# Optimization experiments

Hardware: AMD Instinct MI355X
Metric: run time of the kernel (lower is better)

Reference implementation:

```python
import jax, jax.numpy as jnp
import numpy as np

CH = 64          # channels
OC = 64          # out_channels
B, H, W = 8, 128, 128
NCA_C = CH + OC  # 128, NCA state channels
K = 3            # kernel_size
DILS = (1, 2, 4, 8)
HID = 64         # NCA update hidden
EPS = 1e-5


def setup_inputs() -> dict:
    key = jax.random.key(0)
    ks = jax.random.split(key, 16)
    def n(k, shape, s=0.02):
        return jax.random.normal(k, shape, jnp.float32) * s
    return {
        "x": jax.random.normal(ks[0], (B, H, W, CH), jnp.float32),
        "c": jax.random.normal(ks[1], (B, OC), jnp.float32),
        # Attention params
        "Wq": n(ks[2], (CH, OC)), "bq": jnp.zeros((OC,), jnp.float32),
        "Wk": n(ks[3], (OC, OC)), "bk": jnp.zeros((OC,), jnp.float32),
        "Wv": n(ks[4], (OC, OC)), "bv": jnp.zeros((OC,), jnp.float32),
        "Wo": n(ks[5], (OC, OC)), "bo": jnp.zeros((OC,), jnp.float32),
        "ln_g": jnp.ones((OC,), jnp.float32), "ln_b": jnp.zeros((OC,), jnp.float32),
        # NCA depthwise perception kernels, one per dilation: [4, NCA_C, 1, K, K]
        "pk": n(ks[6], (len(DILS), NCA_C, 1, K, K), 0.1),
        # NCA update MLP
        "W1": n(ks[7], ((1 + len(DILS)) * NCA_C, HID)), "b1": jnp.zeros((HID,), jnp.float32),
        "W2": n(ks[8], (HID, CH)), "b2": jnp.zeros((CH,), jnp.float32),
    }


def _layernorm(z, g, b):
    m = jnp.mean(z, axis=-1, keepdims=True)
    v = jnp.var(z, axis=-1, keepdims=True)
    return (z - m) / jnp.sqrt(v + EPS) * g + b


def _forward(x, c, Wq, bq, Wk, bk, Wv, bv, Wo, bo, ln_g, ln_b, pk, W1, b1, W2, b2):
    b_, h_, w_, _ = x.shape
    # ---- Attention(x, c): single-key softmax pooling over H*W ----
    q = x.reshape(b_, h_ * w_, CH) @ Wq + bq              # [B, HW, OC]
    k = c @ Wk + bk                                        # [B, OC]
    v = c @ Wv + bv                                        # [B, OC]
    scores = jnp.einsum('bno,bo->bn', q, k) * (OC ** -0.5)  # [B, HW]
    attn = jax.nn.softmax(scores, axis=1)                  # softmax over spatial dim
    attended = jnp.einsum('bn,bo->bo', attn, v)            # weighted pool (weights sum to 1)
    a = _layernorm(attended @ Wo + bo + c, ln_g, ln_b)     # out_proj + residual + LN
    c2 = c + a                                             # outer residual in NCAAttention

    # ---- concat broadcast context -> NCA state [B,H,W,NCA_C] ----
    c_exp = jnp.broadcast_to(c2[:, None, None, :], (b_, h_, w_, OC))
    xc = jnp.concatenate([x, c_exp], axis=-1)

    # ---- NCA perception: depthwise dilated convs (SAME padding) ----
    xp = jnp.transpose(xc, (0, 3, 1, 2))                   # NCHW
    feats = [xc]
    for i, d in enumerate(DILS):
        pad = d * (K // 2)
        p = jax.lax.conv_general_dilated(
            xp, pk[i], window_strides=(1, 1),
            padding=[(pad, pad), (pad, pad)], rhs_dilation=(d, d),
            dimension_numbers=('NCHW', 'OIHW', 'NCHW'),
            feature_group_count=NCA_C)
        feats.append(jnp.transpose(p, (0, 2, 3, 1)))
    upd_in = jnp.concatenate(feats, axis=-1)               # [B,H,W,5*NCA_C]

    # ---- NCA update MLP: Linear -> (Dropout=id) -> GELU -> Linear ----
    hidden = jax.nn.gelu(upd_in @ W1 + b1, approximate=False)
    y = hidden @ W2 + b2                                   # [B,H,W,CH]
    # NCA.out_channels (64) != NCA.channels (128) -> no residual add
    return y, c2


def reference(x, c, Wq, bq, Wk, bk, Wv, bv, Wo, bo, ln_g, ln_b, pk, W1, b1, W2, b2):
    return _forward(x, c, Wq, bq, Wk, bk, Wv, bv, Wo, bo, ln_g, ln_b, pk, W1, b1, W2, b2)
```

## Files before the change

### kernel.cpp

```cpp
#include <hip/hip_runtime.h>
#include <hip/hip_bf16.h>
#include <math.h>


typedef float  f32x4 __attribute__((ext_vector_type(4)));
typedef short  s16x8 __attribute__((ext_vector_type(8)));
typedef long   i64x2 __attribute__((ext_vector_type(2)));

static __device__ __forceinline__ unsigned short f2bf(float f) {
    __hip_bfloat16 h = __float2bfloat16(f);
    unsigned short u; __builtin_memcpy(&u, &h, 2); return u;
}
static __device__ __forceinline__ unsigned pk4fp8(float f0, float f1, float f2, float f3) {
    int v = 0;
    v = __builtin_amdgcn_cvt_pk_fp8_f32(f0, f1, v, false);
    v = __builtin_amdgcn_cvt_pk_fp8_f32(f2, f3, v, true);
    return (unsigned)v;
}

#define XROWB  9216
#define XBATCH 1327104
#define USCALE 256.0f

__global__ void prep1(const float* __restrict__ c,
                      const float* __restrict__ Wv, const float* __restrict__ bv,
                      const float* __restrict__ Wo, const float* __restrict__ bo,
                      const float* __restrict__ lng, const float* __restrict__ lnb,
                      float* __restrict__ c2f, float* __restrict__ outc2)
{
    const int b = blockIdx.x, j = threadIdx.x;
    __shared__ float sc[64], sv[64];
    float cj = c[b*64 + j];
    sc[j] = cj; __syncthreads();
    float v = bv[j];
    for (int i = 0; i < 64; ++i) v += sc[i]*Wv[i*64 + j];
    sv[j] = v; __syncthreads();
    float t = bo[j] + cj;
    for (int i = 0; i < 64; ++i) t += sv[i]*Wo[i*64 + j];
    float s = t;
    for (int o = 32; o > 0; o >>= 1) s += __shfl_xor(s, o);
    float m = s * (1.f/64.f);
    float dq = (t - m)*(t - m);
    for (int o = 32; o > 0; o >>= 1) dq += __shfl_xor(dq, o);
    float a = (t - m) / sqrtf(dq*(1.f/64.f) + 1e-5f) * lng[j] + lnb[j];
    float c2 = cj + a;
    c2f[b*64 + j] = c2;
    outc2[b*64 + j] = c2;
}

__global__ void prep2(const float* __restrict__ x,  const float* __restrict__ pk,
                      const float* __restrict__ W1, const float* __restrict__ W2,
                      const float* __restrict__ b1, const float* __restrict__ c2f,
                      unsigned char* __restrict__ xp, unsigned char* __restrict__ Uf,
                      unsigned short* __restrict__ W2s,
                      float* __restrict__ V, float* __restrict__ hcp)
{
    const int blk = blockIdx.x, tid = threadIdx.x;
    if (blk < 512) {
        int i = blk*256 + tid;
        int xc = i & 127, y = (i >> 7) & 127, b = i >> 14;
        const float* src = x + (size_t)i*64;
        float4 f[16];
        #pragma unroll
        for (int k = 0; k < 16; ++k) f[k] = *(const float4*)(src + k*4);
        unsigned P[16];
        #pragma unroll
        for (int k = 0; k < 16; ++k) P[k] = pk4fp8(f[k].x, f[k].y, f[k].z, f[k].w);
        unsigned char* d = xp + (size_t)b*XBATCH + (size_t)(y+8)*XROWB + (size_t)(xc+8)*64;
        *(uint4*)(d +  0) = make_uint4(P[0], P[1], P[8],  P[9]);
        *(uint4*)(d + 16) = make_uint4(P[2], P[3], P[10], P[11]);
        *(uint4*)(d + 32) = make_uint4(P[4], P[5], P[12], P[13]);
        *(uint4*)(d + 48) = make_uint4(P[6], P[7], P[14], P[15]);
    } else if (blk < 648) {
        int idx = (blk - 512)*256 + tid;
        int b = idx / 4352, r = idx - b*4352;
        int yy, xx;
        if (r < 2304) { int ry = r / 144; xx = r - ry*144; yy = (ry < 8) ? ry : 128 + ry; }
        else { int r2 = r - 2304; yy = 8 + (r2 >> 4); int xi = r2 & 15; xx = (xi < 8) ? xi : 128 + xi; }
        unsigned char* d = xp + (size_t)b*XBATCH + (size_t)yy*XROWB + (size_t)xx*64;
        uint4 z = make_uint4(0,0,0,0);
        *(uint4*)(d) = z; *(uint4*)(d+16) = z; *(uint4*)(d+32) = z; *(uint4*)(d+48) = z;
    } else if (blk < 681) {
        int idx = (blk - 648)*256 + tid;
        if (idx < 8448) {
            int lane = idx & 63, nt = (idx >> 6) & 3, pos = idx >> 8;
            int n  = nt*16 + (lane & 15);
            static constexpr int DI[33] = {3,3,3, 2,2,2, 1,1,1, 0,0,0, -1, 0,0, 1,1, 2,2, 3,3,
                                           0,0,0, 1,1,1, 2,2,2, 3,3,3};
            static constexpr int TT[33] = {0,1,2, 0,1,2, 0,1,2, 0,1,2, 4, 3,5, 3,5, 3,5, 3,5,
                                           6,7,8, 6,7,8, 6,7,8, 6,7,8};
            int di = DI[pos], t = TT[pos];
            float vv[16];
            #pragma unroll
            for (int kc2 = 0; kc2 < 2; ++kc2)
                #pragma unroll
                for (int j = 0; j < 8; ++j) {
                    int ch = kc2*32 + (lane >> 4)*8 + j;
                    float v;
                    if (di < 0) {
                        v = W1[ch*64 + n];
                        for (int dd = 0; dd < 4; ++dd)
                            v += pk[(dd*128 + ch)*9 + 4] * W1[((1+dd)*128 + ch)*64 + n];
                    } else {
                        v = pk[(di*128 + ch)*9 + t] * W1[((1+di)*128 + ch)*64 + n];
                    }
                    vv[kc2*8 + j] = v * USCALE;
                }
            uint4 o;
            o.x = pk4fp8(vv[0],  vv[1],  vv[2],  vv[3]);
            o.y = pk4fp8(vv[4],  vv[5],  vv[6],  vv[7]);
            o.z = pk4fp8(vv[8],  vv[9],  vv[10], vv[11]);
            o.w = pk4fp8(vv[12], vv[13], vv[14], vv[15]);
            *(uint4*)(Uf + (size_t)idx*16) = o;
        }
    } else if (blk < 683) {
        int idx = (blk - 681)*256 + tid;
        int lane = idx & 63, nt = (idx >> 6) & 3, kc2 = (idx >> 8) & 1;
        int n  = nt*16 + (lane & 15);
        int k0 = kc2*32 + (lane >> 4)*8;
        unsigned short e[8];
        #pragma unroll
        for (int j = 0; j < 8; ++j) e[j] = f2bf(W2[(k0+j)*64 + n]);
        uint4 o;
        o.x = (unsigned)e[0] | ((unsigned)e[1] << 16);
        o.y = (unsigned)e[2] | ((unsigned)e[3] << 16);
        o.z = (unsigned)e[4] | ((unsigned)e[5] << 16);
        o.w = (unsigned)e[6] | ((unsigned)e[7] << 16);
        *(uint4*)(W2s + (size_t)idx*8) = o;
    } else if (blk < 755) {
        int idx = (blk - 683)*256 + tid;
        int n = idx & 63, q = idx >> 6;
        int p = q % 36, b = q / 36;
        int di = p/9, t = p%9;
        float s = 0.f;
        for (int j = 0; j < 64; ++j)
            s += c2f[b*64 + j] * pk[(di*128 + 64 + j)*9 + t] * W1[((1+di)*128 + 64 + j)*64 + n];
        V[(size_t)q*64 + n] = s;
    } else {
        for (int it = tid; it < 512; it += 256) {
            int b = it >> 6, n = it & 63;
            float s = b1[n];
            for (int j = 0; j < 64; ++j) s += c2f[b*64 + j]*W1[(64 + j)*64 + n];
            hcp[it] = s;
        }
    }
}

#define HID_S 72

__global__ __launch_bounds__(256) void nca_main(
    const unsigned char* __restrict__ xp,
    const unsigned char* __restrict__ U,
    const unsigned short* __restrict__ W2s,
    const float* __restrict__ V,
    const float* __restrict__ hcp,
    const float* __restrict__ b2,
    float* __restrict__ out)
{
    __shared__ unsigned short hid[256*HID_S];
    __shared__ float V_l[36*64];
    __shared__ float Cx_l[16*64];
    __shared__ float Cy_l[2*64];
    __shared__ float hc2_l[64];

    const int tid = threadIdx.x;
    const int blk = blockIdx.x;
    const int b  = blk & 7;
    const int y0 = (blk >> 3) * 2;

    {
        const float4* Vg = (const float4*)(V + (size_t)b*2304);
        for (int i = tid; i < 576; i += 256) ((float4*)V_l)[i] = Vg[i];
    }
    __syncthreads();
    for (int it = tid; it < 1024; it += 256) {
        int xi = it >> 6, n = it & 63;
        int xx = xi < 8 ? xi : 112 + xi;
        float s = 0.f;
        #pragma unroll
        for (int di = 0; di < 4; ++di) {
            int d = 1 << di;
            int dxo = (xx < d) ? 0 : ((xx >= 128 - d) ? 2 : -1);
            if (dxo >= 0) {
                s += V_l[(di*9 + 0*3 + dxo)*64 + n];
                s += V_l[(di*9 + 1*3 + dxo)*64 + n];
                s += V_l[(di*9 + 2*3 + dxo)*64 + n];
            }
        }
        Cx_l[it] = s;
    }
    for (int it = tid; it < 128; it += 256) {
        int r = it >> 6, n = it & 63;
        int yy = y0 + r;
        float s = 0.f;
        #pragma unroll
        for (int di = 0; di < 4; ++di) {
            int d = 1 << di;
            int dyo = (yy < d) ? 0 : ((yy >= 128 - d) ? 2 : -1);
            if (dyo >= 0) {
                s += V_l[(di*9 + dyo*3 + 0)*64 + n];
                s += V_l[(di*9 + dyo*3 + 1)*64 + n];
                s += V_l[(di*9 + dyo*3 + 2)*64 + n];
            }
        }
        Cy_l[it] = s;
    }
    if (tid < 64) {
        float s = hcp[b*64 + tid];
        for (int p = 0; p < 36; ++p) s += V_l[p*64 + tid];
        hc2_l[tid] = s;
    }
    __syncthreads();

    const int lane = tid & 63;
    const int w    = tid >> 6;
    const int y    = y0 + (w >> 1);
    const int xw   = (w & 1) * 64;
    const int ln15 = lane & 15;
    const int oct  = lane >> 4;

    const unsigned char* abase = xp + (size_t)b*XBATCH + (size_t)(y + 8)*XROWB
                               + (size_t)(xw + ln15 + 8)*64 + oct*16;
    const unsigned char* ubase = U + (size_t)lane*16;

    f32x4 acc[4][4];
    #pragma unroll
    for (int mt = 0; mt < 4; ++mt)
        #pragma unroll
        for (int nt = 0; nt < 4; ++nt) {
            acc[mt][nt][0] = 0.f; acc[mt][nt][1] = 0.f;
            acc[mt][nt][2] = 0.f; acc[mt][nt][3] = 0.f;
        }

    static constexpr int OFF[33] = {
        (-8*144-8)*64, (-8*144)*64, (-8*144+8)*64,
        (-4*144-4)*64, (-4*144)*64, (-4*144+4)*64,
        (-2*144-2)*64, (-2*144)*64, (-2*144+2)*64,
        (-1*144-1)*64, (-1*144)*64, (-1*144+1)*64,
        0,
        -64, 64, -128, 128, -256, 256, -512, 512,
        ( 1*144-1)*64, ( 1*144)*64, ( 1*144+1)*64,
        ( 2*144-2)*64, ( 2*144)*64, ( 2*144+2)*64,
        ( 4*144-4)*64, ( 4*144)*64, ( 4*144+4)*64,
        ( 8*144-8)*64, ( 8*144)*64, ( 8*144+8)*64
    };

    i64x2 Ac[4], An[4], Bc[4], Bn[4];
    #pragma unroll
    for (int mt = 0; mt < 4; ++mt) Ac[mt] = *(const i64x2*)(abase + OFF[0] + mt*1024);
    #pragma unroll
    for (int nt = 0; nt < 4; ++nt) Bc[nt] = *(const i64x2*)(ubase + nt*1024);

    #pragma unroll 1
    for (int pos = 0; pos < 33; ++pos) {
        if (pos < 32) {
            const unsigned char* rp = abase + OFF[pos + 1];
            #pragma unroll
            for (int mt = 0; mt < 4; ++mt) An[mt] = *(const i64x2*)(rp + mt*1024);
            const unsigned char* up = ubase + (size_t)(pos + 1)*4096;
            #pragma unroll
            for (int nt = 0; nt < 4; ++nt) Bn[nt] = *(const i64x2*)(up + nt*1024);
        }
        #pragma unroll
        for (int kc2 = 0; kc2 < 2; ++kc2) {
            #pragma unroll
            for (int nt = 0; nt < 4; ++nt) {
                long bf = Bc[nt][kc2];
                #pragma unroll
                for (int mt = 0; mt < 4; ++mt)
                    acc[mt][nt] = __builtin_amdgcn_mfma_f32_16x16x32_fp8_fp8(Ac[mt][kc2], bf, acc[mt][nt], 0, 0, 0);
            }
        }
        #pragma unroll
        for (int mt = 0; mt < 4; ++mt) Ac[mt] = An[mt];
        #pragma unroll
        for (int nt = 0; nt < 4; ++nt) Bc[nt] = Bn[nt];
    }

    const bool yedge = (y < 8) || (y >= 120);
    #pragma unroll
    for (int mt = 0; mt < 4; ++mt) {
        #pragma unroll
        for (int nt = 0; nt < 4; ++nt) {
            const int n = nt*16 + ln15;
            const float hcv = hc2_l[n];
            const float cyv = yedge ? Cy_l[(w >> 1)*64 + n] : 0.f;
            #pragma unroll
            for (int r = 0; r < 4; ++r) {
                int m = oct*4 + r;
                int x = xw + mt*16 + m;
                float h = acc[mt][nt][r]*(1.0f/USCALE) + hcv - cyv;
                if (x < 8 || x >= 120) {
                    int xi = (x < 8) ? x : (x - 112);
                    h -= Cx_l[xi*64 + n];
                    if (yedge) {
                        #pragma unroll
                        for (int di = 0; di < 4; ++di) {
                            int d = 1 << di;
                            int dyo = (y < d) ? 0 : ((y >= 128 - d) ? 2 : -1);
                            int dxo = (x < d) ? 0 : ((x >= 128 - d) ? 2 : -1);
                            if (dyo >= 0 && dxo >= 0)
                                h += V_l[(di*9 + dyo*3 + dxo)*64 + n];
                        }
                    }
                }
                float u = 0.7978845608028654f * (h + 0.044715f*h*h*h);
                float g = h / (1.f + __expf(-2.f*u));
                hid[(w*64 + mt*16 + m)*HID_S + n] = f2bf(g);
            }
        }
    }

    f32x4 acc2[4][4];
    #pragma unroll
    for (int mt = 0; mt < 4; ++mt)
        #pragma unroll
        for (int nt = 0; nt < 4; ++nt) {
            acc2[mt][nt][0] = 0.f; acc2[mt][nt][1] = 0.f;
            acc2[mt][nt][2] = 0.f; acc2[mt][nt][3] = 0.f;
        }
    #pragma unroll
    for (int kc2 = 0; kc2 < 2; ++kc2) {
        s16x8 a2[4];
        #pragma unroll
        for (int mt = 0; mt < 4; ++mt)
            a2[mt] = *(const s16x8*)&hid[(w*64 + mt*16 + ln15)*HID_S + kc2*32 + oct*8];
        #pragma unroll
        for (int nt = 0; nt < 4; ++nt) {
            s16x8 bf = *(const s16x8*)(W2s + ((size_t)(kc2*4 + nt)*64 + lane)*8);
            #pragma unroll
            for (int mt = 0; mt < 4; ++mt)
                acc2[mt][nt] = __builtin_amdgcn_mfma_f32_16x16x32_bf16(a2[mt], bf, acc2[mt][nt], 0, 0, 0);
        }
    }

    float* ob = out + ((size_t)(b*128 + y))*128*64;
    #pragma unroll
    for (int nt = 0; nt < 4; ++nt) {
        const float b2v = b2[nt*16 + ln15];
        #pragma unroll
        for (int mt = 0; mt < 4; ++mt) {
            #pragma unroll
            for (int r = 0; r < 4; ++r) {
                int x = xw + mt*16 + oct*4 + r;
                ob[(size_t)x*64 + nt*16 + ln15] = acc2[mt][nt][r] + b2v;
            }
        }
    }
}

extern "C" void kernel_launch(void* const* d_in, const int* in_sizes, int n_in,
                              void* d_out, int out_size, void* d_ws, size_t ws_size,
                              hipStream_t stream) {
    const float* x   = (const float*)d_in[0];
    const float* c   = (const float*)d_in[1];
    const float* Wv  = (const float*)d_in[6];
    const float* bv  = (const float*)d_in[7];
    const float* Wo  = (const float*)d_in[8];
    const float* bo  = (const float*)d_in[9];
    const float* lng = (const float*)d_in[10];
    const float* lnb = (const float*)d_in[11];
    const float* pk  = (const float*)d_in[12];
    const float* W1  = (const float*)d_in[13];
    const float* b1  = (const float*)d_in[14];
    const float* W2  = (const float*)d_in[15];
    const float* b2  = (const float*)d_in[16];
    float* out = (float*)d_out;

    char* w = (char*)d_ws;
    unsigned char*  xpb = (unsigned char*)(w);
    unsigned char*  Uf  = (unsigned char*)(w + 10616832);
    unsigned short* W2s = (unsigned short*)(w + 10752000);
    float*          V   = (float*)         (w + 10760192);
    float*          hcp = (float*)         (w + 10833920);
    float*          c2f = (float*)         (w + 10835968);

    prep1<<<8, 64, 0, stream>>>(c, Wv, bv, Wo, bo, lng, lnb, c2f, out + 8388608);
    prep2<<<757, 256, 0, stream>>>(x, pk, W1, W2, b1, c2f, xpb, Uf, W2s, V, hcp);
    nca_main<<<512, 256, 0, stream>>>(xpb, Uf, W2s, V, hcp, b2, out);
}
```

Before: 162.0 us.

## Fuse attention prep into prep kernel and halve rows per main block

The separate prep1 launch is removed: blocks that need c2 now recompute the attention, LayerNorm and residual redundantly in shared memory, which saves one kernel launch and a dependency. nca_main now handles one image row per block with 32 pixels per wave, doubling the grid to 1024 blocks and setting launch_bounds min blocks to 4 so occupancy can rise. The software pipeline is rewritten as a two-buffer ping-pong to drop the register copies. The cost is redundant small matmuls in about 74 blocks and less work per wave for amortising the B-fragment loads.

```diff
diff --git a/kernel.cpp b/kernel.cpp
--- a/kernel.cpp
+++ b/kernel.cpp
@@ -22,40 +22,50 @@
 #define XBATCH 1327104
 #define USCALE 256.0f
 
-__global__ void prep1(const float* __restrict__ c,
+__global__ void prep2(const float* __restrict__ x,  const float* __restrict__ pk,
+                      const float* __restrict__ W1, const float* __restrict__ W2,
+                      const float* __restrict__ b1,
+                      const float* __restrict__ c,
                       const float* __restrict__ Wv, const float* __restrict__ bv,
                       const float* __restrict__ Wo, const float* __restrict__ bo,
                       const float* __restrict__ lng, const float* __restrict__ lnb,
-                      float* __restrict__ c2f, float* __restrict__ outc2)
-{
-    const int b = blockIdx.x, j = threadIdx.x;
-    __shared__ float sc[64], sv[64];
-    float cj = c[b*64 + j];
-    sc[j] = cj; __syncthreads();
-    float v = bv[j];
-    for (int i = 0; i < 64; ++i) v += sc[i]*Wv[i*64 + j];
-    sv[j] = v; __syncthreads();
-    float t = bo[j] + cj;
-    for (int i = 0; i < 64; ++i) t += sv[i]*Wo[i*64 + j];
-    float s = t;
-    for (int o = 32; o > 0; o >>= 1) s += __shfl_xor(s, o);
-    float m = s * (1.f/64.f);
-    float dq = (t - m)*(t - m);
-    for (int o = 32; o > 0; o >>= 1) dq += __shfl_xor(dq, o);
-    float a = (t - m) / sqrtf(dq*(1.f/64.f) + 1e-5f) * lng[j] + lnb[j];
-    float c2 = cj + a;
-    c2f[b*64 + j] = c2;
-    outc2[b*64 + j] = c2;
-}
-
-__global__ void prep2(const float* __restrict__ x,  const float* __restrict__ pk,
-                      const float* __restrict__ W1, const float* __restrict__ W2,
-                      const float* __restrict__ b1, const float* __restrict__ c2f,
                       unsigned char* __restrict__ xp, unsigned char* __restrict__ Uf,
                       unsigned short* __restrict__ W2s,
-                      float* __restrict__ V, float* __restrict__ hcp)
+                      float* __restrict__ V, float* __restrict__ hcp,
+                      float* __restrict__ outc2)
 {
     const int blk = blockIdx.x, tid = threadIdx.x;
+    __shared__ float sc[512], sv[512], c2s[512];
+
+    if (blk >= 683) {
+        sc[tid] = c[tid]; sc[tid + 256] = c[tid + 256];
+        __syncthreads();
+        #pragma unroll
+        for (int half = 0; half < 2; ++half) {
+            int it = tid + half*256;
+            int bb = it >> 6, j = it & 63;
+            float v = bv[j];
+            for (int i = 0; i < 64; ++i) v += sc[bb*64 + i]*Wv[i*64 + j];
+            sv[it] = v;
+        }
+        __syncthreads();
+        #pragma unroll
+        for (int half = 0; half < 2; ++half) {
+            int it = tid + half*256;
+            int bb = it >> 6, j = it & 63;
+            float t = bo[j] + sc[it];
+            for (int i = 0; i < 64; ++i) t += sv[bb*64 + i]*Wo[i*64 + j];
+            float s = t;
+            for (int o = 32; o > 0; o >>= 1) s += __shfl_xor(s, o);
+            float m = s * (1.f/64.f);
+            float dq = (t - m)*(t - m);
+            for (int o = 32; o > 0; o >>= 1) dq += __shfl_xor(dq, o);
+            float a = (t - m) / sqrtf(dq*(1.f/64.f) + 1e-5f) * lng[j] + lnb[j];
+            c2s[it] = sc[it] + a;
+        }
+        __syncthreads();
+    }
+
     if (blk < 512) {
         int i = blk*256 + tid;
         int xc = i & 127, y = (i >> 7) & 127, b = i >> 14;
@@ -134,21 +144,22 @@
         int di = p/9, t = p%9;
         float s = 0.f;
         for (int j = 0; j < 64; ++j)
-            s += c2f[b*64 + j] * pk[(di*128 + 64 + j)*9 + t] * W1[((1+di)*128 + 64 + j)*64 + n];
+            s += c2s[b*64 + j] * pk[(di*128 + 64 + j)*9 + t] * W1[((1+di)*128 + 64 + j)*64 + n];
         V[(size_t)q*64 + n] = s;
     } else {
         for (int it = tid; it < 512; it += 256) {
             int b = it >> 6, n = it & 63;
             float s = b1[n];
-            for (int j = 0; j < 64; ++j) s += c2f[b*64 + j]*W1[(64 + j)*64 + n];
+            for (int j = 0; j < 64; ++j) s += c2s[b*64 + j]*W1[(64 + j)*64 + n];
             hcp[it] = s;
+            if (blk == 755) outc2[it] = c2s[it];
         }
     }
 }
 
 #define HID_S 72
 
-__global__ __launch_bounds__(256) void nca_main(
+__global__ __launch_bounds__(256, 4) void nca_main(
     const unsigned char* __restrict__ xp,
     const unsigned char* __restrict__ U,
     const unsigned short* __restrict__ W2s,
@@ -157,16 +168,16 @@
     const float* __restrict__ b2,
     float* __restrict__ out)
 {
-    __shared__ unsigned short hid[256*HID_S];
+    __shared__ unsigned short hid[128*HID_S];
     __shared__ float V_l[36*64];
     __shared__ float Cx_l[16*64];
-    __shared__ float Cy_l[2*64];
+    __shared__ float Cy_l[64];
     __shared__ float hc2_l[64];
 
     const int tid = threadIdx.x;
     const int blk = blockIdx.x;
     const int b  = blk & 7;
-    const int y0 = (blk >> 3) * 2;
+    const int y  = blk >> 3;
 
     {
         const float4* Vg = (const float4*)(V + (size_t)b*2304);
@@ -189,33 +200,31 @@
         }
         Cx_l[it] = s;
     }
-    for (int it = tid; it < 128; it += 256) {
-        int r = it >> 6, n = it & 63;
-        int yy = y0 + r;
+    if (tid < 64) {
+        int n = tid;
         float s = 0.f;
         #pragma unroll
         for (int di = 0; di < 4; ++di) {
             int d = 1 << di;
-            int dyo = (yy < d) ? 0 : ((yy >= 128 - d) ? 2 : -1);
+            int dyo = (y < d) ? 0 : ((y >= 128 - d) ? 2 : -1);
             if (dyo >= 0) {
                 s += V_l[(di*9 + dyo*3 + 0)*64 + n];
                 s += V_l[(di*9 + dyo*3 + 1)*64 + n];
                 s += V_l[(di*9 + dyo*3 + 2)*64 + n];
             }
         }
-        Cy_l[it] = s;
-    }
-    if (tid < 64) {
-        float s = hcp[b*64 + tid];
-        for (int p = 0; p < 36; ++p) s += V_l[p*64 + tid];
-        hc2_l[tid] = s;
+        Cy_l[n] = s;
+    } else if (tid < 128) {
+        int n = tid - 64;
+        float s = hcp[b*64 + n];
+        for (int p = 0; p < 36; ++p) s += V_l[p*64 + n];
+        hc2_l[n] = s;
     }
     __syncthreads();
 
     const int lane = tid & 63;
     const int w    = tid >> 6;
-    const int y    = y0 + (w >> 1);
-    const int xw   = (w & 1) * 64;
+    const int xw   = w * 32;
     const int ln15 = lane & 15;
     const int oct  = lane >> 4;
 
@@ -223,9 +232,9 @@
                                + (size_t)(xw + ln15 + 8)*64 + oct*16;
     const unsigned char* ubase = U + (size_t)lane*16;
 
-    f32x4 acc[4][4];
-    #pragma unroll
-    for (int mt = 0; mt < 4; ++mt)
+    f32x4 acc[2][4];
+    #pragma unroll
+    for (int mt = 0; mt < 2; ++mt)
         #pragma unroll
         for (int nt = 0; nt < 4; ++nt) {
             acc[mt][nt][0] = 0.f; acc[mt][nt][1] = 0.f;
@@ -245,46 +254,45 @@
         ( 8*144-8)*64, ( 8*144)*64, ( 8*144+8)*64
     };
 
-    i64x2 Ac[4], An[4], Bc[4], Bn[4];
-    #pragma unroll
-    for (int mt = 0; mt < 4; ++mt) Ac[mt] = *(const i64x2*)(abase + OFF[0] + mt*1024);
-    #pragma unroll
-    for (int nt = 0; nt < 4; ++nt) Bc[nt] = *(const i64x2*)(ubase + nt*1024);
-
+    auto load_AB = [&](int pos, i64x2* A, i64x2* Bv) {
+        const unsigned char* rp = abase + OFF[pos];
+        #pragma unroll
+        for (int mt = 0; mt < 2; ++mt) A[mt] = *(const i64x2*)(rp + mt*1024);
+        const unsigned char* up = ubase + (size_t)pos*4096;
+        #pragma unroll
+        for (int nt = 0; nt < 4; ++nt) Bv[nt] = *(const i64x2*)(up + nt*1024);
+    };
+    auto mfma_step = [&](const i64x2* A, const i64x2* Bv) {
+        #pragma unroll
+        for (int kc2 = 0; kc2 < 2; ++kc2)
+            #pragma unroll
+            for (int nt = 0; nt < 4; ++nt) {
+                long bf = Bv[nt][kc2];
+                #pragma unroll
+                for (int mt = 0; mt < 2; ++mt)
+                    acc[mt][nt] = __builtin_amdgcn_mfma_f32_16x16x32_fp8_fp8(A[mt][kc2], bf, acc[mt][nt], 0, 0, 0);
+            }
+    };
+
+    i64x2 A0[2], A1[2], B0[4], B1[4];
+    load_AB(0, A0, B0);
     #pragma unroll 1
-    for (int pos = 0; pos < 33; ++pos) {
-        if (pos < 32) {
-            const unsigned char* rp = abase + OFF[pos + 1];
-            #pragma unroll
-            for (int mt = 0; mt < 4; ++mt) An[mt] = *(const i64x2*)(rp + mt*1024);
-            const unsigned char* up = ubase + (size_t)(pos + 1)*4096;
-            #pragma unroll
-            for (int nt = 0; nt < 4; ++nt) Bn[nt] = *(const i64x2*)(up + nt*1024);
-        }
-        #pragma unroll
-        for (int kc2 = 0; kc2 < 2; ++kc2) {
-            #pragma unroll
-            for (int nt = 0; nt < 4; ++nt) {
-                long bf = Bc[nt][kc2];
-                #pragma unroll
-                for (int mt = 0; mt < 4; ++mt)
-                    acc[mt][nt] = __builtin_amdgcn_mfma_f32_16x16x32_fp8_fp8(Ac[mt][kc2], bf, acc[mt][nt], 0, 0, 0);
-            }
-        }
-        #pragma unroll
-        for (int mt = 0; mt < 4; ++mt) Ac[mt] = An[mt];
-        #pragma unroll
-        for (int nt = 0; nt < 4; ++nt) Bc[nt] = Bn[nt];
-    }
+    for (int it2 = 0; it2 < 16; ++it2) {
+        load_AB(2*it2 + 1, A1, B1);
+        mfma_step(A0, B0);
+        load_AB(2*it2 + 2, A0, B0);
+        mfma_step(A1, B1);
+    }
+    mfma_step(A0, B0);
 
     const bool yedge = (y < 8) || (y >= 120);
     #pragma unroll
-    for (int mt = 0; mt < 4; ++mt) {
+    for (int mt = 0; mt < 2; ++mt) {
         #pragma unroll
         for (int nt = 0; nt < 4; ++nt) {
             const int n = nt*16 + ln15;
             const float hcv = hc2_l[n];
-            const float cyv = yedge ? Cy_l[(w >> 1)*64 + n] : 0.f;
+            const float cyv = yedge ? Cy_l[n] : 0.f;
             #pragma unroll
             for (int r = 0; r < 4; ++r) {
                 int m = oct*4 + r;
@@ -306,14 +314,14 @@
                 }
                 float u = 0.7978845608028654f * (h + 0.044715f*h*h*h);
                 float g = h / (1.f + __expf(-2.f*u));
-                hid[(w*64 + mt*16 + m)*HID_S + n] = f2bf(g);
-            }
-        }
-    }
-
-    f32x4 acc2[4][4];
-    #pragma unroll
-    for (int mt = 0; mt < 4; ++mt)
+                hid[x*HID_S + n] = f2bf(g);
+            }
+        }
+    }
+
+    f32x4 acc2[2][4];
+    #pragma unroll
+    for (int mt = 0; mt < 2; ++mt)
         #pragma unroll
         for (int nt = 0; nt < 4; ++nt) {
             acc2[mt][nt][0] = 0.f; acc2[mt][nt][1] = 0.f;
@@ -321,15 +329,15 @@
         }
     #pragma unroll
     for (int kc2 = 0; kc2 < 2; ++kc2) {
-        s16x8 a2[4];
-        #pragma unroll
-        for (int mt = 0; mt < 4; ++mt)
-            a2[mt] = *(const s16x8*)&hid[(w*64 + mt*16 + ln15)*HID_S + kc2*32 + oct*8];
+        s16x8 a2[2];
+        #pragma unroll
+        for (int mt = 0; mt < 2; ++mt)
+            a2[mt] = *(const s16x8*)&hid[(xw + mt*16 + ln15)*HID_S + kc2*32 + oct*8];
         #pragma unroll
         for (int nt = 0; nt < 4; ++nt) {
             s16x8 bf = *(const s16x8*)(W2s + ((size_t)(kc2*4 + nt)*64 + lane)*8);
             #pragma unroll
-            for (int mt = 0; mt < 4; ++mt)
+            for (int mt = 0; mt < 2; ++mt)
                 acc2[mt][nt] = __builtin_amdgcn_mfma_f32_16x16x32_bf16(a2[mt], bf, acc2[mt][nt], 0, 0, 0);
         }
     }
@@ -339,7 +347,7 @@
     for (int nt = 0; nt < 4; ++nt) {
         const float b2v = b2[nt*16 + ln15];
         #pragma unroll
-        for (int mt = 0; mt < 4; ++mt) {
+        for (int mt = 0; mt < 2; ++mt) {
             #pragma unroll
             for (int r = 0; r < 4; ++r) {
                 int x = xw + mt*16 + oct*4 + r;
@@ -373,9 +381,8 @@
     unsigned short* W2s = (unsigned short*)(w + 10752000);
     float*          V   = (float*)         (w + 10760192);
     float*          hcp = (float*)         (w + 10833920);
-    float*          c2f = (float*)         (w + 10835968);
-
-    prep1<<<8, 64, 0, stream>>>(c, Wv, bv, Wo, bo, lng, lnb, c2f, out + 8388608);
-    prep2<<<757, 256, 0, stream>>>(x, pk, W1, W2, b1, c2f, xpb, Uf, W2s, V, hcp);
-    nca_main<<<512, 256, 0, stream>>>(xpb, Uf, W2s, V, hcp, b2, out);
-}
+
+    prep2<<<757, 256, 0, stream>>>(x, pk, W1, W2, b1, c, Wv, bv, Wo, bo, lng, lnb,
+                                   xpb, Uf, W2s, V, hcp, out + 8388608);
+    nca_main<<<1024, 256, 0, stream>>>(xpb, Uf, W2s, V, hcp, b2, out);
+}
```

After: 166.7 us. 1.03x slower.
